# Optimization experiments

Hardware: AMD Instinct MI355X
Metric: run time of the kernel (lower is better)

The kernel has to match this reference:

```python
import jax, jax.numpy as jnp
import numpy as np

NEG_INF = -1e10
DIST_THRESH = 0


def _collect_entities(rep, pos, mask):
    # rep: [B, N, H]; pos: [B, M, S] int; mask: [B, M, S] float
    B, M, S = pos.shape
    g = jnp.take_along_axis(rep, pos.reshape(B, M * S)[:, :, None], axis=1)  # [B, M*S, H]
    g = g.reshape(B, M, S, rep.shape[-1]) * mask[..., None]
    return g.sum(axis=2)  # [B, M, H]


def setup_inputs() -> dict:
    key = jax.random.key(0)
    ks = jax.random.split(key, 10)
    B, N, H = 8, 2048, 512
    M, S = 96, 16
    E, D, R, MAXD = 256, 64, 5, 600
    scale = 0.02
    return {
        'node_hidden': jax.random.normal(ks[0], (B, N, H), jnp.float32),
        'chem_map': jax.random.randint(ks[1], (B, M, S), 0, N),
        'chem_mask': jnp.ones((B, M, S), jnp.float32),
        'dis_map': jax.random.randint(ks[2], (B, M, S), 0, N),
        'dis_mask': jnp.ones((B, M, S), jnp.float32),
        'distance': jax.random.randint(ks[3], (B, M, M), 0, MAXD),
        'W_chem': jax.random.normal(ks[4], (H, E), jnp.float32) * scale,
        'b_chem': jnp.zeros((E,), jnp.float32),
        'W_dis': jax.random.normal(ks[5], (H, E), jnp.float32) * scale,
        'b_dis': jnp.zeros((E,), jnp.float32),
        'W_score': jax.random.normal(ks[6], (2 * E + H + D, R), jnp.float32) * scale,
        'b_score': jnp.zeros((R,), jnp.float32),
        'dist_emb': jax.random.normal(ks[7], (MAXD, D), jnp.float32) * scale,
    }


def reference(node_hidden, chem_map, chem_mask, dis_map, dis_mask, distance,
              W_chem, b_chem, W_dis, b_dis, W_score, b_score, dist_emb):
    B, M = chem_map.shape[0], chem_map.shape[1]
    E = W_chem.shape[1]

    # sentence representation: max-pool over tokens  -> [B, H]
    sent = jnp.max(node_hidden, axis=1)

    # gather mention spans, masked sum pool, tanh-linear  -> [B, M, E]
    chem = jnp.tanh(_collect_entities(node_hidden, chem_map, chem_mask) @ W_chem + b_chem)
    dis = jnp.tanh(_collect_entities(node_hidden, dis_map, dis_mask) @ W_dis + b_dis)

    dist_e = dist_emb[distance]  # [B, M, M, D]

    # pairwise concat: [chem_i, dis_j, dist_ij, sent]  -> [B, M, M, 2E+D+H]
    concat = jnp.concatenate([
        jnp.broadcast_to(chem[:, :, None, :], (B, M, M, E)),
        jnp.broadcast_to(dis[:, None, :, :], (B, M, M, E)),
        dist_e,
        jnp.broadcast_to(sent[:, None, None, :], (B, M, M, sent.shape[-1])),
    ], axis=-1)

    score = jnp.einsum('bmnf,fr->bmnr', concat, W_score) + b_score  # [B, M, M, R]

    # validity masks: non-empty spans and distance >= threshold
    chem_valid = chem_mask.sum(axis=-1) > 0  # [B, M]
    dis_valid = dis_mask.sum(axis=-1) > 0    # [B, M]
    pair_valid = chem_valid[:, :, None] & dis_valid[:, None, :]  # [B, M, M]
    valid = pair_valid & (distance >= DIST_THRESH)
    score = jnp.where(valid[..., None], score, NEG_INF)

    # max-pool over all mention pairs  -> [B, R]
    return jnp.max(score.reshape(B, M * M, -1), axis=1)
```

## Files before the change

### kernel.cpp

```cpp
#include <hip/hip_runtime.h>
#include <math.h>

constexpr int B = 8, N = 2048, H = 512, M = 96, S = 16;
constexpr int E = 256, D = 64, R = 5, MAXD = 600;
constexpr int NZ = 64;
constexpr int NCHUNK = N / NZ;
constexpr int MTA = 4;
constexpr int MT4 = 8;
constexpr float NEG_INF = -1e10f;

constexpr int A_GEMM = 2 * B * (M / MTA);
constexpr int A_SENT = 256;
constexpr int A_DIST = MAXD / 4;
constexpr int A_GRID = A_GEMM + A_SENT + A_DIST;

__device__ inline void atomicMaxFloat(float* addr, float val) {
    int* ai = (int*)addr;
    int old = *ai;
    while (__int_as_float(old) < val) {
        int assumed = old;
        old = atomicCAS(ai, assumed, __float_as_int(val));
        if (old == assumed) break;
    }
}

__global__ void kA(const float* __restrict__ node,
                   const int* __restrict__ cmap, const float* __restrict__ cmask,
                   const int* __restrict__ dmap, const float* __restrict__ dmask,
                   const float* __restrict__ Wc, const float* __restrict__ bc,
                   const float* __restrict__ Wd, const float* __restrict__ bd,
                   const float* __restrict__ Wsc, const float* __restrict__ emb,
                   float* __restrict__ part, float* __restrict__ sAB,
                   float* __restrict__ validAB, float* __restrict__ sD,
                   float* __restrict__ out) {
    const int blk = blockIdx.x;
    const int t = threadIdx.x;

    if (blk == 0 && t < B * R) out[t] = NEG_INF;

    if (blk < A_GEMM) {
        int j  = blk;
        int mg = j % (M / MTA);
        int b  = (j / (M / MTA)) % B;
        int z  = j / ((M / MTA) * B);
        const float* W    = z ? Wd : Wc;
        const float* bias = z ? bd : bc;
        const int*   map  = z ? dmap  : cmap;
        const float* mask = z ? dmask : cmask;
        int scoff = z ? E : 0;

        __shared__ float pooled[MTA][H];
        __shared__ float red4[4][MTA][E];
        __shared__ int   smap[MTA][S];
        __shared__ float smask[MTA][S];

        if (t < MTA * S) {
            int mi = t >> 4, s = t & 15;
            size_t off = ((size_t)b * M + mg * MTA + mi) * S + s;
            smap[mi][s]  = map[off];
            smask[mi][s] = mask[off];
        }
        __syncthreads();

        #pragma unroll
        for (int mi = 0; mi < MTA; ++mi) {
            float a0 = 0.f, a1 = 0.f;
            #pragma unroll
            for (int s = 0; s < S; ++s) {
                float mk = smask[mi][s];
                const float2 v = reinterpret_cast<const float2*>(
                    node + ((size_t)b * N + smap[mi][s]) * H)[t];
                a0 += mk * v.x; a1 += mk * v.y;
            }
            reinterpret_cast<float2*>(&pooled[mi][0])[t] = make_float2(a0, a1);
        }
        if (t < MTA) {
            float ms = 0.f;
            #pragma unroll
            for (int s = 0; s < S; ++s) ms += smask[t][s];
            validAB[((size_t)z * B + b) * M + mg * MTA + t] = (ms > 0.f) ? 1.f : 0.f;
        }
        __syncthreads();

        const int eq = t & 63;
        const int w  = t >> 6;
        const int h0 = w * (H / 4);
        const float4* W4 = reinterpret_cast<const float4*>(W) + eq;
        float4 acc[MTA];
        #pragma unroll
        for (int mi = 0; mi < MTA; ++mi) acc[mi] = make_float4(0.f, 0.f, 0.f, 0.f);

        #pragma unroll 8
        for (int hh = 0; hh < H / 4; ++hh) {
            int h = h0 + hh;
            float4 wv = W4[(size_t)h * (E / 4)];
            #pragma unroll
            for (int mi = 0; mi < MTA; ++mi) {
                float p = pooled[mi][h];
                acc[mi].x += p * wv.x; acc[mi].y += p * wv.y;
                acc[mi].z += p * wv.z; acc[mi].w += p * wv.w;
            }
        }
        #pragma unroll
        for (int mi = 0; mi < MTA; ++mi)
            reinterpret_cast<float4*>(&red4[w][mi][0])[eq] = acc[mi];
        __syncthreads();

        {
            const int mi = w;
            float4 dv = reinterpret_cast<const float4*>(&red4[0][mi][0])[eq];
            #pragma unroll
            for (int ww = 1; ww < 4; ++ww) {
                float4 v = reinterpret_cast<const float4*>(&red4[ww][mi][0])[eq];
                dv.x += v.x; dv.y += v.y; dv.z += v.z; dv.w += v.w;
            }
            float4 bv = reinterpret_cast<const float4*>(bias)[eq];
            float v0 = tanhf(dv.x + bv.x);
            float v1 = tanhf(dv.y + bv.y);
            float v2 = tanhf(dv.z + bv.z);
            float v3 = tanhf(dv.w + bv.w);

            int e0 = scoff + 4 * eq;
            float p[R];
            #pragma unroll
            for (int r = 0; r < R; ++r) {
                p[r] = v0 * Wsc[(size_t)(e0 + 0) * R + r] + v1 * Wsc[(size_t)(e0 + 1) * R + r]
                     + v2 * Wsc[(size_t)(e0 + 2) * R + r] + v3 * Wsc[(size_t)(e0 + 3) * R + r];
            }
            #pragma unroll
            for (int r = 0; r < R; ++r) {
                for (int off = 32; off; off >>= 1) p[r] += __shfl_down(p[r], off, 64);
            }
            if (eq == 0) {
                size_t row = ((size_t)z * B + b) * M + mg * MTA + mi;
                #pragma unroll
                for (int r = 0; r < R; ++r) sAB[row * R + r] = p[r];
            }
        }
    } else if (blk < A_GEMM + A_SENT) {
        int sb = blk - A_GEMM;
        int b = sb >> 5;
        int z = ((sb & 31) << 1) + (t >> 7);
        int tt = t & 127;
        const float4* p = reinterpret_cast<const float4*>(
            node + ((size_t)b * N + (size_t)z * NCHUNK) * H) + tt;
        float4 mx = p[0];
        #pragma unroll
        for (int n = 1; n < NCHUNK; ++n) {
            float4 v = p[(size_t)n * (H / 4)];
            mx.x = fmaxf(mx.x, v.x); mx.y = fmaxf(mx.y, v.y);
            mx.z = fmaxf(mx.z, v.z); mx.w = fmaxf(mx.w, v.w);
        }
        reinterpret_cast<float4*>(part + ((size_t)z * B + b) * H)[tt] = mx;
    } else {
        int d = (blk - A_GEMM - A_SENT) * 4 + (t >> 6);
        int k = t & 63;
        float v = emb[(size_t)d * D + k];
        #pragma unroll
        for (int r = 0; r < R; ++r) {
            float p = v * Wsc[(size_t)(2 * E + k) * R + r];
            for (int off = 32; off; off >>= 1) p += __shfl_down(p, off, 64);
            if (k == 0) sD[d * R + r] = p;
        }
    }
}

__global__ void kB(const float* __restrict__ part, const float* __restrict__ Wsc,
                   const float* __restrict__ bsc,
                   const int* __restrict__ distance,
                   const float* __restrict__ sAB, const float* __restrict__ validAB,
                   const float* __restrict__ sD, float* __restrict__ out) {
    const int g = blockIdx.x % (M / MT4);
    const int b = blockIdx.x / (M / MT4);
    const int t = threadIdx.x;

    __shared__ float sent[H];
    __shared__ float red[R][4];
    __shared__ float sSb[R];
    __shared__ float lB[M * R];
    __shared__ float lD[MAXD * R];
    __shared__ float lA[MT4 * R];
    __shared__ float lvA[MT4], lvB[M];

    for (int h = t; h < H; h += 256) {
        float mx = -INFINITY;
        #pragma unroll 8
        for (int z = 0; z < NZ; ++z) mx = fmaxf(mx, part[((size_t)z * B + b) * H + h]);
        sent[h] = mx;
    }
    __syncthreads();

    float acc[R] = {};
    for (int h = t; h < H; h += 256) {
        float v = sent[h];
        const float* w = Wsc + (size_t)(2 * E + D + h) * R;
        #pragma unroll
        for (int r = 0; r < R; ++r) acc[r] += v * w[r];
    }
    int wave = t >> 6, lane = t & 63;
    #pragma unroll
    for (int r = 0; r < R; ++r) {
        float v = acc[r];
        for (int off = 32; off; off >>= 1) v += __shfl_down(v, off, 64);
        if (lane == 0) red[r][wave] = v;
    }
    __syncthreads();
    if (t < R) sSb[t] = red[t][0] + red[t][1] + red[t][2] + red[t][3] + bsc[t];
    __syncthreads();

    for (int i = t; i < M * R; i += 256) lB[i] = sAB[((size_t)(B + b)) * M * R + i];
    for (int i = t; i < MAXD * R; i += 256) lD[i] = sD[i];
    if (t < MT4 * R) lA[t] = sAB[((size_t)b * M + g * MT4) * R + t] + sSb[t % R];
    if (t < MT4) lvA[t] = validAB[(size_t)b * M + g * MT4 + t];
    for (int i = t; i < M; i += 256) lvB[i] = validAB[((size_t)B + b) * M + i];
    __syncthreads();

    float mx[R];
    #pragma unroll
    for (int r = 0; r < R; ++r) mx[r] = NEG_INF;

    #pragma unroll
    for (int it = 0; it < (MT4 * M) / 256; ++it) {
        int idx = it * 256 + t;
        int mi = idx / M, n = idx % M;
        int dist = distance[((size_t)b * M + g * MT4 + mi) * M + n];
        if (lvA[mi] > 0.f && lvB[n] > 0.f && dist >= 0 ) {
            #pragma unroll
            for (int r = 0; r < R; ++r)
                mx[r] = fmaxf(mx[r], lA[mi * R + r] + lB[n * R + r] + lD[dist * R + r]);
        }
    }
    #pragma unroll
    for (int r = 0; r < R; ++r) {
        float v = mx[r];
        for (int off = 32; off; off >>= 1) v = fmaxf(v, __shfl_down(v, off, 64));
        if (lane == 0) red[r][wave] = v;
    }
    __syncthreads();
    if (t < R) {
        float v = fmaxf(fmaxf(red[t][0], red[t][1]), fmaxf(red[t][2], red[t][3]));
        atomicMaxFloat(out + b * R + t, v);
    }
}

extern "C" void kernel_launch(void* const* d_in, const int* in_sizes, int n_in,
                              void* d_out, int out_size, void* d_ws, size_t ws_size,
                              hipStream_t stream) {
    const float* node     = (const float*)d_in[0];
    const int*   cmap     = (const int*)  d_in[1];
    const float* cmask    = (const float*)d_in[2];
    const int*   dmap     = (const int*)  d_in[3];
    const float* dmask    = (const float*)d_in[4];
    const int*   distance = (const int*)  d_in[5];
    const float* Wc       = (const float*)d_in[6];
    const float* bc       = (const float*)d_in[7];
    const float* Wd       = (const float*)d_in[8];
    const float* bd       = (const float*)d_in[9];
    const float* Wsc      = (const float*)d_in[10];
    const float* bsc      = (const float*)d_in[11];
    const float* emb      = (const float*)d_in[12];
    float* out = (float*)d_out;

    float* ws      = (float*)d_ws;
    float* part    = ws;
    float* sAB     = part + (size_t)NZ * B * H;
    float* validAB = sAB + 2 * B * M * R;
    float* sD      = validAB + 2 * B * M;

    hipLaunchKernelGGL(kA, dim3(A_GRID), dim3(256), 0, stream,
                       node, cmap, cmask, dmap, dmask, Wc, bc, Wd, bd, Wsc, emb,
                       part, sAB, validAB, sD, out);
    hipLaunchKernelGGL(kB, dim3((M / MT4) * B), dim3(256), 0, stream,
                       part, Wsc, bsc, distance, sAB, validAB, sD, out);
}
```

Baseline: 60.20 us.

## Increase mentions per block to 6 and vectorize gather and GEMM inner loop

Raises the number of mentions handled per GEMM block from 4 to 6, so each W row load is reused across more mentions and fewer blocks are launched. The span gather now uses float4 loads, with two mentions per pass across the two halves of the block. The projection loop reads four W rows and a float4 of pooled values per step. The epilogue loops over mentions because there are now more mentions than warps, and the larger shared arrays and accumulator count increase register and LDS pressure.

```diff
diff --git a/kernel.cpp b/kernel.cpp
--- a/kernel.cpp
+++ b/kernel.cpp
@@ -5,7 +5,7 @@
 constexpr int E = 256, D = 64, R = 5, MAXD = 600;
 constexpr int NZ = 64;
 constexpr int NCHUNK = N / NZ;
-constexpr int MTA = 4;
+constexpr int MTA = 6;
 constexpr int MT4 = 8;
 constexpr float NEG_INF = -1e10f;
 
@@ -24,15 +24,16 @@
     }
 }
 
-__global__ void kA(const float* __restrict__ node,
-                   const int* __restrict__ cmap, const float* __restrict__ cmask,
-                   const int* __restrict__ dmap, const float* __restrict__ dmask,
-                   const float* __restrict__ Wc, const float* __restrict__ bc,
-                   const float* __restrict__ Wd, const float* __restrict__ bd,
-                   const float* __restrict__ Wsc, const float* __restrict__ emb,
-                   float* __restrict__ part, float* __restrict__ sAB,
-                   float* __restrict__ validAB, float* __restrict__ sD,
-                   float* __restrict__ out) {
+__global__ __launch_bounds__(256)
+void kA(const float* __restrict__ node,
+        const int* __restrict__ cmap, const float* __restrict__ cmask,
+        const int* __restrict__ dmap, const float* __restrict__ dmask,
+        const float* __restrict__ Wc, const float* __restrict__ bc,
+        const float* __restrict__ Wd, const float* __restrict__ bd,
+        const float* __restrict__ Wsc, const float* __restrict__ emb,
+        float* __restrict__ part, float* __restrict__ sAB,
+        float* __restrict__ validAB, float* __restrict__ sD,
+        float* __restrict__ out) {
     const int blk = blockIdx.x;
     const int t = threadIdx.x;
 
@@ -63,16 +64,19 @@
         __syncthreads();
 
         #pragma unroll
-        for (int mi = 0; mi < MTA; ++mi) {
-            float a0 = 0.f, a1 = 0.f;
+        for (int pass = 0; pass < MTA / 2; ++pass) {
+            int mi = pass * 2 + (t >> 7);
+            int tt = t & 127;
+            float4 a = make_float4(0.f, 0.f, 0.f, 0.f);
             #pragma unroll
             for (int s = 0; s < S; ++s) {
                 float mk = smask[mi][s];
-                const float2 v = reinterpret_cast<const float2*>(
-                    node + ((size_t)b * N + smap[mi][s]) * H)[t];
-                a0 += mk * v.x; a1 += mk * v.y;
-            }
-            reinterpret_cast<float2*>(&pooled[mi][0])[t] = make_float2(a0, a1);
+                const float4 v = reinterpret_cast<const float4*>(
+                    node + ((size_t)b * N + smap[mi][s]) * H)[tt];
+                a.x += mk * v.x; a.y += mk * v.y;
+                a.z += mk * v.z; a.w += mk * v.w;
+            }
+            reinterpret_cast<float4*>(&pooled[mi][0])[tt] = a;
         }
         if (t < MTA) {
             float ms = 0.f;
@@ -90,15 +94,20 @@
         #pragma unroll
         for (int mi = 0; mi < MTA; ++mi) acc[mi] = make_float4(0.f, 0.f, 0.f, 0.f);
 
-        #pragma unroll 8
-        for (int hh = 0; hh < H / 4; ++hh) {
-            int h = h0 + hh;
-            float4 wv = W4[(size_t)h * (E / 4)];
+        #pragma unroll 4
+        for (int hh4 = 0; hh4 < (H / 4) / 4; ++hh4) {
+            int h = h0 + hh4 * 4;
+            const float4 w0 = W4[(size_t)(h + 0) * (E / 4)];
+            const float4 w1 = W4[(size_t)(h + 1) * (E / 4)];
+            const float4 w2 = W4[(size_t)(h + 2) * (E / 4)];
+            const float4 w3 = W4[(size_t)(h + 3) * (E / 4)];
             #pragma unroll
             for (int mi = 0; mi < MTA; ++mi) {
-                float p = pooled[mi][h];
-                acc[mi].x += p * wv.x; acc[mi].y += p * wv.y;
-                acc[mi].z += p * wv.z; acc[mi].w += p * wv.w;
+                const float4 p = *reinterpret_cast<const float4*>(&pooled[mi][h]);
+                acc[mi].x += p.x*w0.x + p.y*w1.x + p.z*w2.x + p.w*w3.x;
+                acc[mi].y += p.x*w0.y + p.y*w1.y + p.z*w2.y + p.w*w3.y;
+                acc[mi].z += p.x*w0.z + p.y*w1.z + p.z*w2.z + p.w*w3.z;
+                acc[mi].w += p.x*w0.w + p.y*w1.w + p.z*w2.w + p.w*w3.w;
             }
         }
         #pragma unroll
@@ -106,8 +115,7 @@
             reinterpret_cast<float4*>(&red4[w][mi][0])[eq] = acc[mi];
         __syncthreads();
 
-        {
-            const int mi = w;
+        for (int mi = w; mi < MTA; mi += 4) {
             float4 dv = reinterpret_cast<const float4*>(&red4[0][mi][0])[eq];
             #pragma unroll
             for (int ww = 1; ww < 4; ++ww) {
```

Result: slower. 68.20 us (+13.3%).
